# Optimization experiments

Hardware: AMD Instinct MI355X
Metric: run time of the kernel (lower is better)

Reference implementation:

```python
import jax, jax.numpy as jnp
import numpy as np

B, N, D = 4, 2048, 1024
DF = 4 * D
EPS = 1e-5


def _layernorm(x, w, b):
    mu = jnp.mean(x, axis=-1, keepdims=True)
    var = jnp.mean(jnp.square(x - mu), axis=-1, keepdims=True)
    return (x - mu) * jax.lax.rsqrt(var + EPS) * w + b


def setup_inputs() -> dict:
    key = jax.random.key(0)
    ks = jax.random.split(key, 8)
    x = jax.random.normal(ks[0], (B, N, D), dtype=jnp.float32)
    # conv filter param (torch init is zeros; use small randn for numeric coverage)
    weights = jax.random.normal(ks[1], (1, 1, N), dtype=jnp.float32) * 0.02
    # registered buffer: sqrt(1/(i+1)) per token, shape (1, N, 1)
    scale = jnp.sqrt(1.0 / (jnp.arange(N, dtype=jnp.float32) + 1.0))[None, :, None]
    ln1_w = jnp.ones((D,), jnp.float32)
    ln1_b = jnp.zeros((D,), jnp.float32)
    W1 = jax.random.normal(ks[2], (DF, D), dtype=jnp.float32) * 0.02
    b1 = jnp.zeros((DF,), jnp.float32)
    W2 = jax.random.normal(ks[3], (D, DF), dtype=jnp.float32) * 0.02
    b2 = jnp.zeros((D,), jnp.float32)
    scalar = jax.random.normal(ks[4], (1,), dtype=jnp.float32) * 0.1
    ln2_w = jnp.ones((D,), jnp.float32)
    ln2_b = jnp.zeros((D,), jnp.float32)
    return dict(x=x, weights=weights, scale=scale, ln1_w=ln1_w, ln1_b=ln1_b,
                W1=W1, b1=b1, W2=W2, b2=b2, scalar=scalar, ln2_w=ln2_w, ln2_b=ln2_b)


def reference(x, weights, scale, ln1_w, ln1_b, W1, b1, W2, b2, scalar, ln2_w, ln2_b):
    n = weights.shape[-1]
    # FFT token-mixing conv: operate over token axis. x: (B,N,D) -> (B,D,N)
    xt = jnp.swapaxes(x, -2, -1)
    # real inputs -> rfft/irfft equals real(ifft(fft*fft)) from the torch code
    prod = jnp.fft.rfft(xt, n=2 * n) * jnp.fft.rfft(weights, n=2 * n)
    conv = jnp.fft.irfft(prod, n=2 * n)[..., :n]  # (B,D,N)
    x1 = jnp.swapaxes(conv, -2, -1)               # (B,N,D)
    x1 = _layernorm(x + x1 * scale, ln1_w, ln1_b)
    # GELU MLP (torch F.gelu default = exact erf gelu)
    h = jax.nn.gelu(jnp.einsum('bnd,fd->bnf', x1, W1) + b1, approximate=False)
    mlp = jnp.einsum('bnf,df->bnd', h, W2) + b2
    x2 = _layernorm(x1 + scalar * mlp, ln2_w, ln2_b)
    return x2
```

## Files before the change

### kernel.cpp

```cpp
#include <hip/hip_runtime.h>
#include <cstdint>

typedef float floatx4 __attribute__((ext_vector_type(4)));
typedef float floatx16 __attribute__((ext_vector_type(16)));
typedef int intx8 __attribute__((ext_vector_type(8)));

__device__ __forceinline__ unsigned short f2b(float f) {
  union { float f; unsigned u; } v; v.f = f;
  return (unsigned short)((v.u + 0x7FFFu + ((v.u >> 16) & 1u)) >> 16);
}
__device__ __forceinline__ float b2f(unsigned short h) {
  union { unsigned u; float f; } v; v.u = ((unsigned)h) << 16;
  return v.f;
}

__device__ __forceinline__ void gload_lds16(const void* g, void* l) {
  __builtin_amdgcn_global_load_lds(
      (const __attribute__((address_space(1))) void*)g,
      (__attribute__((address_space(3))) void*)l, 16, 0, 0);
}

__device__ __forceinline__ intx8 lds_read32s(const unsigned char* base,
                                             int lo, int hi) {
  union { intx8 v; int4 q[2]; } u;
  u.q[0] = *(const int4*)(base + lo);
  u.q[1] = *(const int4*)(base + hi);
  return u.v;
}

__device__ __forceinline__ int swz_scol(int lane) {
  return (((lane & 7) ^ ((lane >> 3) & 7)) << 4);
}

__global__ __launch_bounds__(256) void prep_kernel(
    const float* __restrict__ W1, const float* __restrict__ W2,
    const float* __restrict__ wconv, const float* __restrict__ x,
    int* __restrict__ W1f8, int* __restrict__ W2f8,
    int* __restrict__ T8, unsigned char* __restrict__ xT) {
  const int bid = blockIdx.x;
  const int tid = threadIdx.x;
  if (bid < 8192) {
    const float* in = (bid < 4096) ? W1 : W2;
    int* out = (bid < 4096) ? W1f8 : W2f8;
    long i = (long)(bid & 4095) * 256 + tid;
    float4 v = ((const float4*)in)[i];
    int pk = __builtin_amdgcn_cvt_pk_fp8_f32(v.x * 64.0f, v.y * 64.0f, 0, false);
    pk = __builtin_amdgcn_cvt_pk_fp8_f32(v.z * 64.0f, v.w * 64.0f, pk, true);
    out[i] = pk;
  } else if (bid < 12288) {
    long i = (long)(bid - 8192) * 256 + tid;
    int n = (int)(i >> 9);
    int m0 = (int)(i & 511) * 4;
    float v[4];
#pragma unroll
    for (int r = 0; r < 4; ++r) {
      int m = m0 + r;
      v[r] = (m <= n) ? wconv[n - m] * 64.0f : 0.0f;
    }
    int pk = __builtin_amdgcn_cvt_pk_fp8_f32(v[0], v[1], 0, false);
    pk = __builtin_amdgcn_cvt_pk_fp8_f32(v[2], v[3], pk, true);
    T8[i] = pk;
  } else {
    __shared__ float tile[32][33];
    const int t = bid - 12288;
    const int d0 = (t & 31) * 32;
    const int n0 = ((t >> 5) & 63) * 32;
    const int b = t >> 11;
    const int tx = tid & 31;
    const int ty = tid >> 5;
    for (int i = ty; i < 32; i += 8)
      tile[i][tx] = x[((long)b * 2048 + n0 + i) * 1024 + d0 + tx];
    __syncthreads();
    float a = tile[ty * 4 + 0][tx];
    float c = tile[ty * 4 + 1][tx];
    float e = tile[ty * 4 + 2][tx];
    float f = tile[ty * 4 + 3][tx];
    int pk = __builtin_amdgcn_cvt_pk_fp8_f32(a, c, 0, false);
    pk = __builtin_amdgcn_cvt_pk_fp8_f32(e, f, pk, true);
    *(int*)(xT + ((long)b * 1024 + d0 + tx) * 2048 + n0 + ty * 4) = pk;
  }
}

template <int EPI, int NT, bool TRI>
__global__ __launch_bounds__(256, 4) void gemm_f8(
    const unsigned char* __restrict__ A, const unsigned char* __restrict__ B,
    int Kstride, int Kloop, long zsA, long zsB, long zsC, long zsP,
    int rx, int ryb, int gxn, unsigned sclA, unsigned sclB,
    const float* __restrict__ bias,
    unsigned short* __restrict__ Cb, unsigned char* __restrict__ C8) {
  __shared__ __align__(16) unsigned char As[16 * 1024];
  __shared__ __align__(16) unsigned char Bs[16 * 1024];
  const int tid = threadIdx.x;
  const int wid = tid >> 6;
  const int lane = tid & 63;
  const int l32 = lane & 31;
  const int half = lane >> 5;
  const int wm = (wid >> 1) * 64;
  const int wn = (wid & 1) * 64;

  const int bid = blockIdx.x;
  const int xcd = bid & 7;
  const int ib = bid >> 3;
  long bm, bn;
  int kstart, kend;
  long pofs = 0;
  if (TRI) {
    const int ci = ib & 7;
    const int ri = (ib >> 3) & 1;
    const int sp = ib >> 4;
    bm = (long)(ri == 0 ? xcd : 15 - xcd) * 128;
    bn = (long)ci * 128;
    const int T = (int)(bm >> 7) + 1;
    const int h = (T + 1) >> 1;
    kstart = (sp ? h : 0) * 128;
    kend = (sp ? T : h) * 128;
    pofs = (long)sp * zsP;
  } else {
    const int ci = ib % rx;
    const int ri = ib / rx;
    const int gx = xcd % gxn;
    const int gy = xcd / gxn;
    bm = (long)(gy * ryb + ri) * 128;
    bn = (long)(gx * rx + ci) * 128;
    kstart = 0;
    kend = Kloop;
  }
  const int bz = blockIdx.z;
  const unsigned char* Ab = A + zsA * bz;
  const unsigned char* Bb = B + zsB * bz;

  floatx16 acc[2][2];
#pragma unroll
  for (int i = 0; i < 2; ++i)
#pragma unroll
    for (int j = 0; j < 2; ++j)
#pragma unroll
      for (int e = 0; e < 16; ++e) acc[i][j][e] = 0.0f;

  const int srow = tid >> 3;
  const int scol = swz_scol(lane);
  const unsigned char* gA[4];
  const unsigned char* gB[4];
  unsigned char* lA[4];
  unsigned char* lB[4];
#pragma unroll
  for (int p = 0; p < 4; ++p) {
    gA[p] = Ab + (bm + p * 32 + srow) * (long)Kstride + scol;
    gB[p] = Bb + (bn + p * 32 + srow) * (long)Kstride + scol;
    lA[p] = As + (p * 4 + wid) * 1024;
    lB[p] = Bs + (p * 4 + wid) * 1024;
  }

  int offA_lo[2][2], offA_hi[2][2], offB_lo[2][2], offB_hi[2][2];
#pragma unroll
  for (int i = 0; i < 2; ++i)
#pragma unroll
    for (int s = 0; s < 2; ++s) {
      const int q0 = s * 4 + half * 2;
      const int ra = (int)wm + i * 32 + l32;
      const int baseA = ra * 128;
      offA_lo[i][s] = baseA + ((q0 ^ (ra & 7)) << 4);
      offA_hi[i][s] = baseA + (((q0 + 1) ^ (ra & 7)) << 4);
      const int rb = (int)wn + i * 32 + l32;
      const int baseB = rb * 128;
      offB_lo[i][s] = baseB + ((q0 ^ (rb & 7)) << 4);
      offB_hi[i][s] = baseB + (((q0 + 1) ^ (rb & 7)) << 4);
    }

  for (int kk = kstart; kk < kend; kk += 128) {
    __syncthreads();
#pragma unroll
    for (int p = 0; p < 4; ++p) {
      gload_lds16(gA[p] + kk, lA[p]);
      gload_lds16(gB[p] + kk, lB[p]);
    }
    __syncthreads();
#pragma unroll
    for (int s = 0; s < 2; ++s) {
      intx8 b0 = lds_read32s(Bs, offB_lo[0][s], offB_hi[0][s]);
      intx8 b1 = lds_read32s(Bs, offB_lo[1][s], offB_hi[1][s]);
      intx8 a0 = lds_read32s(As, offA_lo[0][s], offA_hi[0][s]);
      intx8 a1 = lds_read32s(As, offA_lo[1][s], offA_hi[1][s]);
      acc[0][0] = __builtin_amdgcn_mfma_scale_f32_32x32x64_f8f6f4(
          a0, b0, acc[0][0], 0, 0, 0, sclA, 0, sclB);
      acc[0][1] = __builtin_amdgcn_mfma_scale_f32_32x32x64_f8f6f4(
          a0, b1, acc[0][1], 0, 0, 0, sclA, 0, sclB);
      acc[1][0] = __builtin_amdgcn_mfma_scale_f32_32x32x64_f8f6f4(
          a1, b0, acc[1][0], 0, 0, 0, sclA, 0, sclB);
      acc[1][1] = __builtin_amdgcn_mfma_scale_f32_32x32x64_f8f6f4(
          a1, b1, acc[1][1], 0, 0, 0, sclA, 0, sclB);
    }
  }

#pragma unroll
  for (int i = 0; i < 2; ++i)
#pragma unroll
    for (int j = 0; j < 2; ++j)
#pragma unroll
      for (int r = 0; r < 16; ++r) {
        long row = bm + wm + i * 32 + (r & 3) + 8 * (r >> 2) + 4 * half;
        long col = bn + wn + j * 32 + l32;
        long idx = pofs + (long)bz * zsC + row * (long)NT + col;
        float v = acc[i][j][r];
        if (EPI == 0) {
          Cb[idx] = f2b(v);
        } else {
          v += bias[col];
          float u = v * (0.7978845608f + 0.0356774081f * v * v);
          float u2 = u * u;
          float t = __fdividef(u * (15.0f + u2), 15.0f + 6.0f * u2);
          t = fminf(fmaxf(t, -1.0f), 1.0f);
          float g = 0.5f * v * (1.0f + t);
          int pk = __builtin_amdgcn_cvt_pk_fp8_f32(g, 0.0f, 0, false);
          C8[idx] = (unsigned char)(pk & 0xFF);
        }
      }
}

__global__ __launch_bounds__(256) void ln1_kernel(
    const float* __restrict__ x, const unsigned short* __restrict__ c0,
    const unsigned short* __restrict__ c1, const float* __restrict__ scale,
    const float* __restrict__ w, const float* __restrict__ b,
    unsigned short* __restrict__ outb, int* __restrict__ outf8) {
  const long row = blockIdx.x;
  const int tid = threadIdx.x;
  float4 xv = ((const float4*)x)[row * 256 + tid];
  ushort4 a4 = ((const ushort4*)c0)[row * 256 + tid];
  ushort4 e4 = ((const ushort4*)c1)[row * 256 + tid];
  const float sc = scale[row & 2047];
  float4 v;
  v.x = xv.x + sc * (b2f(a4.x) + b2f(e4.x));
  v.y = xv.y + sc * (b2f(a4.y) + b2f(e4.y));
  v.z = xv.z + sc * (b2f(a4.z) + b2f(e4.z));
  v.w = xv.w + sc * (b2f(a4.w) + b2f(e4.w));
  float s = v.x + v.y + v.z + v.w;
  float ss = v.x * v.x + v.y * v.y + v.z * v.z + v.w * v.w;
#pragma unroll
  for (int off = 32; off > 0; off >>= 1) {
    s += __shfl_down(s, off);
    ss += __shfl_down(ss, off);
  }
  __shared__ float red[8];
  const int wid = tid >> 6, lane = tid & 63;
  if (lane == 0) { red[wid] = s; red[4 + wid] = ss; }
  __syncthreads();
  s = red[0] + red[1] + red[2] + red[3];
  ss = red[4] + red[5] + red[6] + red[7];
  const float mu = s * (1.0f / 1024.0f);
  const float var = ss * (1.0f / 1024.0f) - mu * mu;
  const float rs = rsqrtf(var + 1e-5f);
  float4 wv = ((const float4*)w)[tid];
  float4 bv = ((const float4*)b)[tid];
  float o0 = (v.x - mu) * rs * wv.x + bv.x;
  float o1 = (v.y - mu) * rs * wv.y + bv.y;
  float o2 = (v.z - mu) * rs * wv.z + bv.z;
  float o3 = (v.w - mu) * rs * wv.w + bv.w;
  ushort4 u{f2b(o0), f2b(o1), f2b(o2), f2b(o3)};
  ((ushort4*)outb)[row * 256 + tid] = u;
  int pk = __builtin_amdgcn_cvt_pk_fp8_f32(o0, o1, 0, false);
  pk = __builtin_amdgcn_cvt_pk_fp8_f32(o2, o3, pk, true);
  outf8[row * 256 + tid] = pk;
}

__global__ __launch_bounds__(256) void ln2_fused_kernel(
    const unsigned short* __restrict__ y0, const unsigned short* __restrict__ y1,
    const unsigned short* __restrict__ x1b, const float* __restrict__ b2,
    const float* __restrict__ scalar_p, const float* __restrict__ w,
    const float* __restrict__ b, float* __restrict__ out) {
  const long row = blockIdx.x;
  const int tid = threadIdx.x;
  ushort4 a4 = ((const ushort4*)y0)[row * 256 + tid];
  ushort4 c4 = ((const ushort4*)y1)[row * 256 + tid];
  ushort4 xr = ((const ushort4*)x1b)[row * 256 + tid];
  float4 bias = ((const float4*)b2)[tid];
  const float scl = scalar_p[0];
  float4 v;
  v.x = b2f(xr.x) + scl * (b2f(a4.x) + b2f(c4.x) + bias.x);
  v.y = b2f(xr.y) + scl * (b2f(a4.y) + b2f(c4.y) + bias.y);
  v.z = b2f(xr.z) + scl * (b2f(a4.z) + b2f(c4.z) + bias.z);
  v.w = b2f(xr.w) + scl * (b2f(a4.w) + b2f(c4.w) + bias.w);
  float s = v.x + v.y + v.z + v.w;
  float ss = v.x * v.x + v.y * v.y + v.z * v.z + v.w * v.w;
#pragma unroll
  for (int off = 32; off > 0; off >>= 1) {
    s += __shfl_down(s, off);
    ss += __shfl_down(ss, off);
  }
  __shared__ float red[8];
  const int wid = tid >> 6, lane = tid & 63;
  if (lane == 0) { red[wid] = s; red[4 + wid] = ss; }
  __syncthreads();
  s = red[0] + red[1] + red[2] + red[3];
  ss = red[4] + red[5] + red[6] + red[7];
  const float mu = s * (1.0f / 1024.0f);
  const float var = ss * (1.0f / 1024.0f) - mu * mu;
  const float rs = rsqrtf(var + 1e-5f);
  float4 wv = ((const float4*)w)[tid];
  float4 bv = ((const float4*)b)[tid];
  float4 o;
  o.x = (v.x - mu) * rs * wv.x + bv.x;
  o.y = (v.y - mu) * rs * wv.y + bv.y;
  o.z = (v.z - mu) * rs * wv.z + bv.z;
  o.w = (v.w - mu) * rs * wv.w + bv.w;
  ((float4*)out)[row * 256 + tid] = o;
}

extern "C" void kernel_launch(void* const* d_in, const int* in_sizes, int n_in,
                              void* d_out, int out_size, void* d_ws, size_t ws_size,
                              hipStream_t stream) {
  const float* x      = (const float*)d_in[0];
  const float* wconv  = (const float*)d_in[1];
  const float* scale  = (const float*)d_in[2];
  const float* ln1w   = (const float*)d_in[3];
  const float* ln1b   = (const float*)d_in[4];
  const float* W1     = (const float*)d_in[5];
  const float* b1     = (const float*)d_in[6];
  const float* W2     = (const float*)d_in[7];
  const float* b2     = (const float*)d_in[8];
  const float* scalar = (const float*)d_in[9];
  const float* ln2w   = (const float*)d_in[10];
  const float* ln2b   = (const float*)d_in[11];
  float* out = (float*)d_out;

  const unsigned SCL_1  = 0x7F7F7F7Fu;
  const unsigned SCL_64 = 0x79797979u;

  char* ws = (char*)d_ws;
  unsigned char* xT8   = (unsigned char*)ws;  ws += (size_t)4 * 1024 * 2048;
  unsigned char* T8    = (unsigned char*)ws;  ws += (size_t)2048 * 2048;
  unsigned char* W1f8  = (unsigned char*)ws;  ws += (size_t)4096 * 1024;
  unsigned char* W2f8  = (unsigned char*)ws;  ws += (size_t)4096 * 1024;
  float* y             = (float*)ws;          ws += (size_t)8192 * 1024 * 4;
  unsigned short* yb   = (unsigned short*)ws; ws += (size_t)2 * 8192 * 1024 * 2;
  unsigned short* x1b  = (unsigned short*)ws; ws += (size_t)8192 * 1024 * 2;
  unsigned char* x1f8  = (unsigned char*)ws;  ws += (size_t)8192 * 1024;
  unsigned char* h8    = (unsigned char*)ws;  ws += (size_t)8192 * 4096;
  (void)y;

  prep_kernel<<<20480, 256, 0, stream>>>(W1, W2, wconv, x,
                                         (int*)W1f8, (int*)W2f8, (int*)T8, xT8);

  gemm_f8<0, 1024, true><<<dim3(256, 1, 4), 256, 0, stream>>>(
      T8, xT8, 2048, 2048, 0L, (long)1024 * 2048, (long)2048 * 1024,
      (long)8192 * 1024, 8, 0, 0, SCL_64, SCL_1, nullptr, yb, nullptr);
  ln1_kernel<<<8192, 256, 0, stream>>>(
      x, yb, yb + (size_t)8192 * 1024, scale, ln1w, ln1b, x1b, (int*)x1f8);
  gemm_f8<2, 4096, false><<<dim3(2048, 1, 1), 256, 0, stream>>>(
      x1f8, W1f8, 1024, 1024, 0L, 0L, 0L, 0L,
      16, 16, 2, SCL_1, SCL_64, b1, nullptr, h8);
  gemm_f8<0, 1024, false><<<dim3(512, 1, 2), 256, 0, stream>>>(
      h8, W2f8, 4096, 2048, 2048L, 2048L, (long)8192 * 1024, 0L,
      8, 8, 1, SCL_1, SCL_64, nullptr, yb, nullptr);
  ln2_fused_kernel<<<8192, 256, 0, stream>>>(
      yb, yb + (size_t)8192 * 1024, x1b, b2, scalar, ln2w, ln2b, out);
}
```

Measured before the change: 283.3 us.

## Add 256x256-tile FP8 GEMM kernel with triple-buffered LDS for MLP GEMMs

Introduces a new 512-thread GEMM kernel that computes 256x256 output tiles per block, with each wave owning a 128x64 sub-tile. Operands stream through a three-stage LDS ring filled by direct global-to-LDS loads, using a narrower 64-byte row swizzle. Both MLP GEMMs (W1 with the GELU epilogue and the split-K W2) switch to it, which raises operand reuse per byte loaded and cuts the number of blocks. The cost is more registers and LDS per block, lower occupancy, and fewer blocks to spread across the CUs.

```diff
diff --git a/kernel.cpp b/kernel.cpp
--- a/kernel.cpp
+++ b/kernel.cpp
@@ -26,10 +26,6 @@
   u.q[0] = *(const int4*)(base + lo);
   u.q[1] = *(const int4*)(base + hi);
   return u.v;
-}
-
-__device__ __forceinline__ int swz_scol(int lane) {
-  return (((lane & 7) ^ ((lane >> 3) & 7)) << 4);
 }
 
 __global__ __launch_bounds__(256) void prep_kernel(
@@ -138,7 +134,7 @@
       for (int e = 0; e < 16; ++e) acc[i][j][e] = 0.0f;
 
   const int srow = tid >> 3;
-  const int scol = swz_scol(lane);
+  const int scol = (((lane & 7) ^ ((lane >> 3) & 7)) << 4);
   const unsigned char* gA[4];
   const unsigned char* gB[4];
   unsigned char* lA[4];
@@ -202,6 +198,169 @@
         long col = bn + wn + j * 32 + l32;
         long idx = pofs + (long)bz * zsC + row * (long)NT + col;
         float v = acc[i][j][r];
+        if (EPI == 0) {
+          Cb[idx] = f2b(v);
+        } else {
+          v += bias[col];
+          float u = v * (0.7978845608f + 0.0356774081f * v * v);
+          float u2 = u * u;
+          float t = __fdividef(u * (15.0f + u2), 15.0f + 6.0f * u2);
+          t = fminf(fmaxf(t, -1.0f), 1.0f);
+          float g = 0.5f * v * (1.0f + t);
+          int pk = __builtin_amdgcn_cvt_pk_fp8_f32(g, 0.0f, 0, false);
+          C8[idx] = (unsigned char)(pk & 0xFF);
+        }
+      }
+}
+
+template <int EPI, int NT>
+__global__ __launch_bounds__(512, 2) void gemm256_f8(
+    const unsigned char* __restrict__ A, const unsigned char* __restrict__ B,
+    int Kstride, int Kloop, long zsA, long zsB, long zsC,
+    int rx, int ryb, int gxn, unsigned sclA, unsigned sclB,
+    const float* __restrict__ bias,
+    unsigned short* __restrict__ Cb, unsigned char* __restrict__ C8) {
+  __shared__ __align__(16) unsigned char As[3 * 16384];
+  __shared__ __align__(16) unsigned char Bs[3 * 16384];
+  const int tid = threadIdx.x;
+  const int wid = tid >> 6;
+  const int lane = tid & 63;
+  const int l32 = lane & 31;
+  const int half = lane >> 5;
+  const int wm = (wid >> 2) * 128;
+  const int wn = (wid & 3) * 64;
+
+  const int bid = blockIdx.x;
+  const int xcd = bid & 7;
+  const int ib = bid >> 3;
+  const int ci = ib % rx;
+  const int ri = ib / rx;
+  const int gx = xcd % gxn;
+  const int gy = xcd / gxn;
+  const long bm = (long)(gy * ryb + ri) * 256;
+  const long bn = (long)(gx * rx + ci) * 256;
+  const int bz = blockIdx.z;
+  const unsigned char* Ab = A + zsA * bz;
+  const unsigned char* Bb = B + zsB * bz;
+
+  floatx16 acc[4][2];
+#pragma unroll
+  for (int i = 0; i < 4; ++i)
+#pragma unroll
+    for (int j = 0; j < 2; ++j)
+#pragma unroll
+      for (int e = 0; e < 16; ++e) acc[i][j][e] = 0.0f;
+
+  const int srow = wid * 16 + (lane >> 2);
+  const int scol = (((lane & 3) ^ ((lane >> 2) & 3)) << 4);
+  const unsigned char* gA[2];
+  const unsigned char* gB[2];
+  int lA[2], lB[2];
+#pragma unroll
+  for (int p = 0; p < 2; ++p) {
+    gA[p] = Ab + (bm + p * 128 + srow) * (long)Kstride + scol;
+    gB[p] = Bb + (bn + p * 128 + srow) * (long)Kstride + scol;
+    lA[p] = (p * 128 + wid * 16) * 64;
+    lB[p] = lA[p];
+  }
+
+  int oAl[4], oAh[4], oBl[2], oBh[2];
+#pragma unroll
+  for (int mi = 0; mi < 4; ++mi) {
+    const int ra = wm + mi * 32 + l32;
+    const int q0 = half * 2;
+    oAl[mi] = ra * 64 + ((q0 ^ (ra & 3)) << 4);
+    oAh[mi] = ra * 64 + (((q0 + 1) ^ (ra & 3)) << 4);
+  }
+#pragma unroll
+  for (int nj = 0; nj < 2; ++nj) {
+    const int rb = wn + nj * 32 + l32;
+    const int q0 = half * 2;
+    oBl[nj] = rb * 64 + ((q0 ^ (rb & 3)) << 4);
+    oBh[nj] = rb * 64 + (((q0 + 1) ^ (rb & 3)) << 4);
+  }
+
+  const int nst = Kloop >> 6;
+
+#pragma unroll
+  for (int p = 0; p < 2; ++p) {
+    gload_lds16(gA[p], As + lA[p]);
+    gload_lds16(gB[p], Bs + lB[p]);
+  }
+#pragma unroll
+  for (int p = 0; p < 2; ++p) {
+    gload_lds16(gA[p] + 64, As + 16384 + lA[p]);
+    gload_lds16(gB[p] + 64, Bs + 16384 + lB[p]);
+  }
+
+  int b = 0, b2 = 2;
+  for (int k = 0; k < nst; ++k) {
+    if (k + 1 < nst) {
+      asm volatile("s_waitcnt vmcnt(4)" ::: "memory");
+    } else {
+      asm volatile("s_waitcnt vmcnt(0)" ::: "memory");
+    }
+    __builtin_amdgcn_s_barrier();
+    const unsigned char* Al = As + b * 16384;
+    const unsigned char* Bl = Bs + b * 16384;
+    const bool pre = (k + 2) < nst;
+    const int kc2 = (k + 2) << 6;
+
+    intx8 bf0 = lds_read32s(Bl, oBl[0], oBh[0]);
+    intx8 bf1 = lds_read32s(Bl, oBl[1], oBh[1]);
+    intx8 a0 = lds_read32s(Al, oAl[0], oAh[0]);
+    intx8 a1 = lds_read32s(Al, oAl[1], oAh[1]);
+    if (pre) {
+      gload_lds16(gA[0] + kc2, As + b2 * 16384 + lA[0]);
+      gload_lds16(gA[1] + kc2, As + b2 * 16384 + lA[1]);
+    }
+    asm volatile("s_waitcnt lgkmcnt(0)" ::: "memory");
+    __builtin_amdgcn_sched_barrier(0);
+    __builtin_amdgcn_s_setprio(1);
+    acc[0][0] = __builtin_amdgcn_mfma_scale_f32_32x32x64_f8f6f4(
+        a0, bf0, acc[0][0], 0, 0, 0, sclA, 0, sclB);
+    acc[0][1] = __builtin_amdgcn_mfma_scale_f32_32x32x64_f8f6f4(
+        a0, bf1, acc[0][1], 0, 0, 0, sclA, 0, sclB);
+    acc[1][0] = __builtin_amdgcn_mfma_scale_f32_32x32x64_f8f6f4(
+        a1, bf0, acc[1][0], 0, 0, 0, sclA, 0, sclB);
+    acc[1][1] = __builtin_amdgcn_mfma_scale_f32_32x32x64_f8f6f4(
+        a1, bf1, acc[1][1], 0, 0, 0, sclA, 0, sclB);
+    __builtin_amdgcn_s_setprio(0);
+    __builtin_amdgcn_s_barrier();
+
+    a0 = lds_read32s(Al, oAl[2], oAh[2]);
+    a1 = lds_read32s(Al, oAl[3], oAh[3]);
+    if (pre) {
+      gload_lds16(gB[0] + kc2, Bs + b2 * 16384 + lB[0]);
+      gload_lds16(gB[1] + kc2, Bs + b2 * 16384 + lB[1]);
+    }
+    asm volatile("s_waitcnt lgkmcnt(0)" ::: "memory");
+    __builtin_amdgcn_sched_barrier(0);
+    __builtin_amdgcn_s_setprio(1);
+    acc[2][0] = __builtin_amdgcn_mfma_scale_f32_32x32x64_f8f6f4(
+        a0, bf0, acc[2][0], 0, 0, 0, sclA, 0, sclB);
+    acc[2][1] = __builtin_amdgcn_mfma_scale_f32_32x32x64_f8f6f4(
+        a0, bf1, acc[2][1], 0, 0, 0, sclA, 0, sclB);
+    acc[3][0] = __builtin_amdgcn_mfma_scale_f32_32x32x64_f8f6f4(
+        a1, bf0, acc[3][0], 0, 0, 0, sclA, 0, sclB);
+    acc[3][1] = __builtin_amdgcn_mfma_scale_f32_32x32x64_f8f6f4(
+        a1, bf1, acc[3][1], 0, 0, 0, sclA, 0, sclB);
+    __builtin_amdgcn_s_setprio(0);
+
+    b = (b == 2) ? 0 : b + 1;
+    b2 = (b2 == 2) ? 0 : b2 + 1;
+  }
+
+#pragma unroll
+  for (int mi = 0; mi < 4; ++mi)
+#pragma unroll
+    for (int nj = 0; nj < 2; ++nj)
+#pragma unroll
+      for (int r = 0; r < 16; ++r) {
+        long row = bm + wm + mi * 32 + (r & 3) + 8 * (r >> 2) + 4 * half;
+        long col = bn + wn + nj * 32 + l32;
+        long idx = (long)bz * zsC + row * (long)NT + col;
+        float v = acc[mi][nj][r];
         if (EPI == 0) {
           Cb[idx] = f2b(v);
         } else {
@@ -345,12 +504,12 @@
       (long)8192 * 1024, 8, 0, 0, SCL_64, SCL_1, nullptr, yb, nullptr);
   ln1_kernel<<<8192, 256, 0, stream>>>(
       x, yb, yb + (size_t)8192 * 1024, scale, ln1w, ln1b, x1b, (int*)x1f8);
-  gemm_f8<2, 4096, false><<<dim3(2048, 1, 1), 256, 0, stream>>>(
-      x1f8, W1f8, 1024, 1024, 0L, 0L, 0L, 0L,
-      16, 16, 2, SCL_1, SCL_64, b1, nullptr, h8);
-  gemm_f8<0, 1024, false><<<dim3(512, 1, 2), 256, 0, stream>>>(
-      h8, W2f8, 4096, 2048, 2048L, 2048L, (long)8192 * 1024, 0L,
-      8, 8, 1, SCL_1, SCL_64, nullptr, yb, nullptr);
+  gemm256_f8<2, 4096><<<dim3(512, 1, 1), 512, 0, stream>>>(
+      x1f8, W1f8, 1024, 1024, 0L, 0L, 0L,
+      8, 8, 2, SCL_1, SCL_64, b1, nullptr, h8);
+  gemm256_f8<0, 1024><<<dim3(128, 1, 2), 512, 0, stream>>>(
+      h8, W2f8, 4096, 2048, 2048L, 2048L, (long)8192 * 1024,
+      4, 4, 1, SCL_1, SCL_64, nullptr, yb, nullptr);
   ln2_fused_kernel<<<8192, 256, 0, stream>>>(
       yb, yb + (size_t)8192 * 1024, x1b, b2, scalar, ln2w, ln2b, out);
 }
```

Result: slower. 299.4 us (+5.7%).
